# Performance work log

Hardware: AMD Instinct MI355X
Metric: run time of the kernel (lower is better)

The kernel has to match this reference:

```python
import jax, jax.numpy as jnp
import numpy as np

B, N, C, M = 64, 8732, 21, 16  # batch, priors (SSD300), classes (VOC), max objects


def setup_inputs() -> dict:
    key = jax.random.key(0)
    k1, k2 = jax.random.split(key)
    confOut = jax.random.normal(k1, (B, N, C), dtype=jnp.float32)
    bboxOut = jax.random.normal(k2, (B, N, 4), dtype=jnp.float32)

    rng = np.random.default_rng(0)
    # prior boxes [x1,y1,x2,y2], positive width/height
    px1 = rng.uniform(0.0, 0.8, (N, 1)).astype(np.float32)
    py1 = rng.uniform(0.0, 0.8, (N, 1)).astype(np.float32)
    pw = rng.uniform(0.05, 0.2, (N, 1)).astype(np.float32)
    ph = rng.uniform(0.05, 0.2, (N, 1)).astype(np.float32)
    predBoxes = np.concatenate([px1, py1, px1 + pw, py1 + ph], axis=1)

    # target layout: [num, (cls,x1,y1,x2,y2,k) * M]
    target = np.zeros((B, 1 + 6 * M), dtype=np.float32)
    target[:, 0] = rng.integers(1, M + 1, B)
    cls = rng.integers(1, C, (B, M)).astype(np.float32)  # all positive classes
    tx1 = rng.uniform(0.0, 0.8, (B, M)).astype(np.float32)
    ty1 = rng.uniform(0.0, 0.8, (B, M)).astype(np.float32)
    tw = rng.uniform(0.05, 0.2, (B, M)).astype(np.float32)
    th = rng.uniform(0.05, 0.2, (B, M)).astype(np.float32)
    ks = np.stack([rng.choice(N, M, replace=False) for _ in range(B)]).astype(np.float32)
    flat = np.stack([cls, tx1, ty1, tx1 + tw, ty1 + th, ks], axis=-1).reshape(B, 6 * M)
    target[:, 1:] = flat

    return {"confOut": confOut, "bboxOut": bboxOut,
            "target": jnp.asarray(target), "predBoxes": jnp.asarray(predBoxes)}


def _encode_box(true_box, pred_box):
    # standard SSD center/size encoding: (tc-pc)/pw, log(tw/pw)
    tcx = (true_box[..., 0] + true_box[..., 2]) * 0.5
    tcy = (true_box[..., 1] + true_box[..., 3]) * 0.5
    tw = true_box[..., 2] - true_box[..., 0]
    th = true_box[..., 3] - true_box[..., 1]
    pcx = (pred_box[..., 0] + pred_box[..., 2]) * 0.5
    pcy = (pred_box[..., 1] + pred_box[..., 3]) * 0.5
    pw = pred_box[..., 2] - pred_box[..., 0]
    ph = pred_box[..., 3] - pred_box[..., 1]
    return jnp.stack([(tcx - pcx) / pw, (tcy - pcy) / ph,
                      jnp.log(tw / pw), jnp.log(th / ph)], axis=-1)


def _ssd_loss(confOut, bboxOut, target, predBoxes):
    b, n, c = confOut.shape
    m = (target.shape[1] - 1) // 6
    t = target[:, 1:1 + 6 * m].reshape(b, m, 6)
    cls = t[..., 0].astype(jnp.int32)          # [B,M]
    tbox = t[..., 1:5]                          # [B,M,4]
    k = t[..., 5].astype(jnp.int32)             # [B,M] prior index
    num = target[:, 0].astype(jnp.int32)        # [B]
    valid = jnp.arange(m)[None, :] < num[:, None]      # [B,M]
    pos = valid & (cls > 0)
    bi = jnp.broadcast_to(jnp.arange(b)[:, None], (b, m))

    # ---- conf target assignment (scatter per object onto prior grid) ----
    posmask = jnp.zeros((b, n), bool).at[bi, k].max(pos)
    assigned = jnp.zeros((b, n), bool).at[bi, k].max(valid)  # score zeroed for all assigned
    conf_cls = jnp.zeros((b, n), jnp.int32).at[bi, k].max(jnp.where(pos, cls, 0))
    pnum = jnp.sum(pos)

    # ---- hard negative mining: globally sort bg log-prob ascending ----
    logp = jax.nn.log_softmax(confOut, axis=-1)             # [B,N,C]
    bg = jnp.where(assigned, 0.0, logp[..., 0]).reshape(-1)  # assigned -> 0 (sorts last)
    order = jnp.argsort(bg)
    pos_sorted = posmask.reshape(-1)[order]
    hit_pos = jnp.cumsum(pos_sorted.astype(jnp.int32)) > 0   # early-break emulation
    sel_sorted = (jnp.arange(b * n) < 3 * pnum) & (~hit_pos)
    negmask = jnp.zeros(b * n, bool).at[order].set(sel_sorted).reshape(b, n)

    selmask = posmask | negmask
    ce = -jnp.take_along_axis(logp, conf_cls[..., None], axis=-1)[..., 0]  # [B,N]
    conf_loss = jnp.sum(jnp.where(selmask, ce, 0.0)) / jnp.maximum(jnp.sum(selmask), 1)

    # ---- bbox target assignment + SmoothL1 on positives ----
    ebox = _encode_box(tbox, predBoxes[k])                   # [B,M,4]
    btgt = jnp.zeros((b, n, 4)).at[bi, k].add(jnp.where(valid[..., None], ebox, 0.0))
    bmask = jnp.zeros((b, n), bool).at[bi, k].max(valid)
    d = bboxOut - btgt
    ad = jnp.abs(d)
    sl1 = jnp.where(ad < 1.0, 0.5 * d * d, ad - 0.5)
    denom = jnp.maximum(jnp.sum(bmask) * 4, 1)
    bbox_loss = jnp.sum(jnp.where(bmask[..., None], sl1, 0.0)) / denom
    return conf_loss, bbox_loss


def reference(confOut, bboxOut, target, predBoxes):
    return _ssd_loss(confOut, bboxOut, target, predBoxes)
```

## Files before the change

### kernel.cpp

```cpp
#include <hip/hip_runtime.h>

constexpr int B = 64, N = 8732, C = 21, M = 16;
constexpr int TROW = 1 + 6 * M;
constexpr int NBIN = 2048;
constexpr unsigned BASE16 = 15103u;
constexpr int NSLAB = 8;
constexpr int TILE = 128;
constexpr int NTILES = (N + TILE - 1) / TILE;
constexpr int BPB = 16;
constexpr float FSCALE = 262144.0f;
constexpr unsigned long long CNT1 = 1ull << 44;
constexpr unsigned long long FIXMASK = (1ull << 44) - 1;

__device__ __forceinline__ unsigned f2key(float f) {
  unsigned u = __float_as_uint(f);
  return (u & 0x80000000u) ? ~u : (u | 0x80000000u);
}
__device__ __forceinline__ float key2f(unsigned k) {
  unsigned u = (k & 0x80000000u) ? (k ^ 0x80000000u) : ~k;
  return __uint_as_float(u);
}

__global__ __launch_bounds__(256) void k_zero(unsigned long long* __restrict__ z) {
  int idx = blockIdx.x * 256 + threadIdx.x;
  z[idx] = 0ull;
}

__global__ __launch_bounds__(256) void k_logp(
    const float* __restrict__ conf, const float* __restrict__ bbox,
    const float* __restrict__ target, const float* __restrict__ pred,
    unsigned long long* __restrict__ slab1, float4* __restrict__ batchCtl) {
  __shared__ __align__(16) float sbuf[2][TILE * C];
  __shared__ unsigned long long shist[NBIN];
  __shared__ int sk[M];
  int b = blockIdx.y, bx = blockIdx.x, tid = threadIdx.x;

  for (int i = tid; i < NBIN; i += 256) shist[i] = 0ull;
  const float* tr = target + (size_t)b * TROW;
  if (tid < M) {
    int num = (int)tr[0];
    sk[tid] = (tid < num) ? (int)tr[1 + 6 * tid + 5] : -1;
  }

  const size_t cbase = (size_t)b * N;
  int nt = (NTILES - 1 - bx) / BPB + 1;

  uint4 r0, r1, r2;
  int ld_nf4 = 0;

#define LOAD_T(kt)                                                        \
  {                                                                       \
    int tt_ = bx + (kt) * BPB;                                            \
    int n0_ = tt_ * TILE;                                                 \
    int rows_ = min(TILE, N - n0_);                                       \
    ld_nf4 = (rows_ * C) >> 2;                                            \
    const uint4* g4_ = (const uint4*)(conf + (cbase + n0_) * C);          \
    if (tid < ld_nf4) r0 = g4_[tid];                                      \
    if (tid + 256 < ld_nf4) r1 = g4_[tid + 256];                          \
    if (tid + 512 < ld_nf4) r2 = g4_[tid + 512];                          \
  }

#define WRITE_T(bi)                                                       \
  {                                                                       \
    uint4* s4_ = (uint4*)sbuf[bi];                                        \
    if (tid < ld_nf4) s4_[tid] = r0;                                      \
    if (tid + 256 < ld_nf4) s4_[tid + 256] = r1;                          \
    if (tid + 512 < ld_nf4) s4_[tid + 512] = r2;                          \
  }

  LOAD_T(0);
  WRITE_T(0);
  __syncthreads();

  for (int t = 0; t < nt; ++t) {
    if (t + 1 < nt) LOAD_T(t + 1);
    {
      int tt_ = bx + t * BPB;
      int n0_ = tt_ * TILE;
      int rows_ = min(TILE, N - n0_);
      if (tid < rows_) {
        int n = n0_ + tid;
        const float* x = sbuf[t & 1] + tid * C;
        float s0 = __expf(x[0]) + __expf(x[4]) + __expf(x[8]) + __expf(x[12]) + __expf(x[16]);
        float s1 = __expf(x[1]) + __expf(x[5]) + __expf(x[9]) + __expf(x[13]) + __expf(x[17]);
        float s2 = __expf(x[2]) + __expf(x[6]) + __expf(x[10]) + __expf(x[14]) + __expf(x[18]);
        float s3 = __expf(x[3]) + __expf(x[7]) + __expf(x[11]) + __expf(x[15]) + __expf(x[19]);
        float s = (s0 + s1) + (s2 + s3) + __expf(x[20]);
        float lp = x[0] - __logf(s);
        bool asg = false;
        for (int j = 0; j < M; j++) asg |= (sk[j] == n);
        if (!asg) {
          int idx = ((int)(f2key(lp) >> 16) - (int)BASE16) >> 1;
          idx = min(max(idx, 0), NBIN - 1);
          atomicAdd(&shist[idx],
                    CNT1 | (unsigned long long)((-lp) * FSCALE + 0.5f));
        }
      }
    }
    if (t + 1 < nt) WRITE_T((t + 1) & 1);
    __syncthreads();
  }
#undef LOAD_T
#undef WRITE_T

  unsigned long long* sg = slab1 + (size_t)(bx & (NSLAB - 1)) * NBIN;
  for (int i = tid; i < NBIN; i += 256) {
    unsigned long long v = shist[i];
    if (v) atomicAdd(&sg[i], v);
  }

  if (bx == 0) {
    float myValid = 0.f, myPos = 0.f, myCE = 0.f, mySL = 0.f;
    if (tid < M && sk[tid] >= 0) {
      const float* e = tr + 1 + 6 * tid;
      int cls = (int)e[0];
      float tx1 = e[1], ty1 = e[2], tx2 = e[3], ty2 = e[4];
      int k = sk[tid];
      float p0 = pred[k * 4 + 0], p1 = pred[k * 4 + 1];
      float p2 = pred[k * 4 + 2], p3 = pred[k * 4 + 3];
      float pw = p2 - p0, ph = p3 - p1;
      float pcx = (p0 + p2) * 0.5f, pcy = (p1 + p3) * 0.5f;
      float tw = tx2 - tx1, th = ty2 - ty1;
      float tcx = (tx1 + tx2) * 0.5f, tcy = (ty1 + ty2) * 0.5f;
      float ebv[4];
      ebv[0] = (tcx - pcx) / pw;
      ebv[1] = (tcy - pcy) / ph;
      ebv[2] = __logf(tw / pw);
      ebv[3] = __logf(th / ph);
      const float* bo = bbox + ((size_t)b * N + k) * 4;
      float sl = 0.f;
      for (int j = 0; j < 4; j++) {
        float d = bo[j] - ebv[j];
        float ad = fabsf(d);
        sl += (ad < 1.f) ? 0.5f * d * d : ad - 0.5f;
      }
      myValid = 1.f; mySL = sl;
      if (cls > 0) {
        const float* x = conf + ((size_t)b * N + k) * C;
        float s = 0.f;
        for (int c = 0; c < C; c++) s += __expf(x[c]);
        float lp = x[cls] - __logf(s);
        myPos = 1.f; myCE = -lp;
      }
    }
    if (tid < 64) {
      for (int off = 32; off; off >>= 1) {
        myValid += __shfl_down(myValid, off, 64);
        myPos   += __shfl_down(myPos, off, 64);
        myCE    += __shfl_down(myCE, off, 64);
        mySL    += __shfl_down(mySL, off, 64);
      }
      if (tid == 0) batchCtl[b] = make_float4(myPos, myValid, myCE, mySL);
    }
  }
}

__global__ __launch_bounds__(1024) void k_fin(
    const unsigned long long* __restrict__ slab1,
    const float4* __restrict__ batchCtl, float* __restrict__ out) {
  __shared__ unsigned long long sm[NBIN];
  __shared__ unsigned long long sscan[1024];
  __shared__ unsigned srank;
  __shared__ float sp, sva, sce, ssl;
  __shared__ double sNeg;
  int tid = threadIdx.x;

  if (tid < 64) {
    float4 v = batchCtl[tid];
    float p = v.x, va = v.y, ce = v.z, sl = v.w;
    for (int off = 32; off; off >>= 1) {
      p  += __shfl_down(p, off, 64);
      va += __shfl_down(va, off, 64);
      ce += __shfl_down(ce, off, 64);
      sl += __shfl_down(sl, off, 64);
    }
    if (tid == 0) {
      sp = p; sva = va; sce = ce; ssl = sl;
      srank = 3u * (unsigned)(p + 0.5f);
      sNeg = 0.0;
    }
  }

  for (int k = 0; k < NBIN / 1024; k++) {
    int bin = tid + k * 1024;
    unsigned long long v = 0ull;
    for (int s = 0; s < NSLAB; s++) v += slab1[(size_t)s * NBIN + bin];
    sm[bin] = v;
  }
  __syncthreads();

  unsigned long long h2[2];
  unsigned long long part = 0ull;
  for (int j = 0; j < 2; j++) { h2[j] = sm[tid * 2 + j]; part += h2[j]; }
  sscan[tid] = part;
  __syncthreads();
  for (int off = 1; off < 1024; off <<= 1) {
    unsigned long long add = (tid >= off) ? sscan[tid - off] : 0ull;
    __syncthreads();
    sscan[tid] += add;
    __syncthreads();
  }

  unsigned rank = srank;
  if (rank) {
    unsigned long long cum = sscan[tid] - part;
    for (int j = 0; j < 2; j++) {
      unsigned long long h = h2[j];
      unsigned c0 = (unsigned)(cum >> 44);
      unsigned c1 = (unsigned)((cum + h) >> 44);
      if (c0 < rank && c1 >= rank) {
        unsigned t = (unsigned)(tid * 2 + j);
        unsigned r = rank - c0;
        unsigned long long fixBelow = cum & FIXMASK;
        float ceEdge = -key2f((BASE16 + 2u * t) << 16);
        sNeg = (double)fixBelow / 262144.0 + (double)r * (double)ceEdge;
      }
      cum += h;
    }
  }
  __syncthreads();
  if (tid == 0) {
    out[0] = (sce + (float)sNeg) / fmaxf(4.0f * sp, 1.0f);
    out[1] = ssl / fmaxf(4.0f * sva, 1.0f);
  }
}

extern "C" void kernel_launch(void* const* d_in, const int* in_sizes, int n_in,
                              void* d_out, int out_size, void* d_ws, size_t ws_size,
                              hipStream_t stream) {
  const float* conf = (const float*)d_in[0];
  const float* bbox = (const float*)d_in[1];
  const float* target = (const float*)d_in[2];
  const float* pred = (const float*)d_in[3];
  float* out = (float*)d_out;

  char* ws = (char*)d_ws;
  unsigned long long* slab1 = (unsigned long long*)ws;
  size_t off = (size_t)NSLAB * NBIN * 8;
  float4* batchCtl = (float4*)(ws + off); off += 64 * 16;

  k_zero<<<64, 256, 0, stream>>>(slab1);
  k_logp<<<dim3(BPB, B), 256, 0, stream>>>(conf, bbox, target, pred,
                                           slab1, batchCtl);
  k_fin<<<1, 1024, 0, stream>>>(slab1, batchCtl, out);
}
```

Before: 31.39 us.

## Double tile size and prefetch two tiles ahead with dual register sets

Tiles grow from 128 to 256 priors, and blocks per batch drop from 16 to 8. The register prefetch becomes two alternating register sets, so global loads run two tiles ahead of compute instead of one. The goal is to hide global-memory latency on the conf stream. In exchange, shared memory doubles (2x256x21 floats), register pressure rises to 12 uint4 per thread, and the grid halves to 512 blocks. Only 256 threads run the softmax while a tile holds 256 rows, so every thread is busy, but occupancy may drop.

```diff
diff --git a/kernel.cpp b/kernel.cpp
--- a/kernel.cpp
+++ b/kernel.cpp
@@ -5,9 +5,9 @@
 constexpr int NBIN = 2048;
 constexpr unsigned BASE16 = 15103u;
 constexpr int NSLAB = 8;
-constexpr int TILE = 128;
+constexpr int TILE = 256;
 constexpr int NTILES = (N + TILE - 1) / TILE;
-constexpr int BPB = 16;
+constexpr int BPB = 8;
 constexpr float FSCALE = 262144.0f;
 constexpr unsigned long long CNT1 = 1ull << 44;
 constexpr unsigned long long FIXMASK = (1ull << 44) - 1;
@@ -45,35 +45,46 @@
   const size_t cbase = (size_t)b * N;
   int nt = (NTILES - 1 - bx) / BPB + 1;
 
-  uint4 r0, r1, r2;
-  int ld_nf4 = 0;
-
-#define LOAD_T(kt)                                                        \
+  uint4 a0, a1, a2, a3, a4, a5;
+  uint4 b0, b1, b2, b3, b4, b5;
+  int la = 0, lb = 0;
+
+#define LOAD_SET(R0, R1, R2, R3, R4, R5, LN, kt)                          \
   {                                                                       \
     int tt_ = bx + (kt) * BPB;                                            \
     int n0_ = tt_ * TILE;                                                 \
     int rows_ = min(TILE, N - n0_);                                       \
-    ld_nf4 = (rows_ * C) >> 2;                                            \
+    LN = (rows_ * C) >> 2;                                                \
     const uint4* g4_ = (const uint4*)(conf + (cbase + n0_) * C);          \
-    if (tid < ld_nf4) r0 = g4_[tid];                                      \
-    if (tid + 256 < ld_nf4) r1 = g4_[tid + 256];                          \
-    if (tid + 512 < ld_nf4) r2 = g4_[tid + 512];                          \
-  }
-
-#define WRITE_T(bi)                                                       \
+    if (tid < LN) R0 = g4_[tid];                                          \
+    if (tid + 256 < LN) R1 = g4_[tid + 256];                              \
+    if (tid + 512 < LN) R2 = g4_[tid + 512];                              \
+    if (tid + 768 < LN) R3 = g4_[tid + 768];                              \
+    if (tid + 1024 < LN) R4 = g4_[tid + 1024];                            \
+    if (tid + 1280 < LN) R5 = g4_[tid + 1280];                            \
+  }
+
+#define WRITE_SET(R0, R1, R2, R3, R4, R5, LN, bi)                         \
   {                                                                       \
     uint4* s4_ = (uint4*)sbuf[bi];                                        \
-    if (tid < ld_nf4) s4_[tid] = r0;                                      \
-    if (tid + 256 < ld_nf4) s4_[tid + 256] = r1;                          \
-    if (tid + 512 < ld_nf4) s4_[tid + 512] = r2;                          \
-  }
-
-  LOAD_T(0);
-  WRITE_T(0);
+    if (tid < LN) s4_[tid] = R0;                                          \
+    if (tid + 256 < LN) s4_[tid + 256] = R1;                              \
+    if (tid + 512 < LN) s4_[tid + 512] = R2;                              \
+    if (tid + 768 < LN) s4_[tid + 768] = R3;                              \
+    if (tid + 1024 < LN) s4_[tid + 1024] = R4;                            \
+    if (tid + 1280 < LN) s4_[tid + 1280] = R5;                            \
+  }
+
+  LOAD_SET(a0, a1, a2, a3, a4, a5, la, 0);
+  WRITE_SET(a0, a1, a2, a3, a4, a5, la, 0);
+  if (1 < nt) LOAD_SET(b0, b1, b2, b3, b4, b5, lb, 1);
   __syncthreads();
 
   for (int t = 0; t < nt; ++t) {
-    if (t + 1 < nt) LOAD_T(t + 1);
+    if (t + 2 < nt) {
+      if ((t & 1) == 0) { LOAD_SET(a0, a1, a2, a3, a4, a5, la, t + 2); }
+      else              { LOAD_SET(b0, b1, b2, b3, b4, b5, lb, t + 2); }
+    }
     {
       int tt_ = bx + t * BPB;
       int n0_ = tt_ * TILE;
@@ -97,11 +108,14 @@
         }
       }
     }
-    if (t + 1 < nt) WRITE_T((t + 1) & 1);
+    if (t + 1 < nt) {
+      if (((t + 1) & 1) == 0) { WRITE_SET(a0, a1, a2, a3, a4, a5, la, 0); }
+      else                    { WRITE_SET(b0, b1, b2, b3, b4, b5, lb, 1); }
+    }
     __syncthreads();
   }
-#undef LOAD_T
-#undef WRITE_T
+#undef LOAD_SET
+#undef WRITE_SET
 
   unsigned long long* sg = slab1 + (size_t)(bx & (NSLAB - 1)) * NBIN;
   for (int i = tid; i < NBIN; i += 256) {
```

Result: faster. 28.42 us (-9.5%).

## Stage conf tiles via direct global-to-LDS loads with larger tiles

Applied to the files above, without the earlier changes.

Replaces register-staged global loads plus LDS writes with __builtin_amdgcn_global_load_lds 16-byte direct copies into the double buffer. Tile size doubles to 256 rows, so every thread computes a row, and blocks per batch drop to 8. The aim is to cut VGPR pressure and the explicit LDS write pass. It relies on the 16-byte LDS-DMA variant being supported and on the syncthreads waiting for the async loads to finish. Fewer blocks (512 instead of 1024) may reduce the parallelism available for latency hiding.

```diff
diff --git a/kernel.cpp b/kernel.cpp
--- a/kernel.cpp
+++ b/kernel.cpp
@@ -5,12 +5,15 @@
 constexpr int NBIN = 2048;
 constexpr unsigned BASE16 = 15103u;
 constexpr int NSLAB = 8;
-constexpr int TILE = 128;
+constexpr int TILE = 256;
 constexpr int NTILES = (N + TILE - 1) / TILE;
-constexpr int BPB = 16;
+constexpr int BPB = 8;
 constexpr float FSCALE = 262144.0f;
 constexpr unsigned long long CNT1 = 1ull << 44;
 constexpr unsigned long long FIXMASK = (1ull << 44) - 1;
+
+typedef __attribute__((address_space(1))) const unsigned int g_as_t;
+typedef __attribute__((address_space(3))) unsigned int l_as_t;
 
 __device__ __forceinline__ unsigned f2key(float f) {
   unsigned u = __float_as_uint(f);
@@ -34,6 +37,7 @@
   __shared__ unsigned long long shist[NBIN];
   __shared__ int sk[M];
   int b = blockIdx.y, bx = blockIdx.x, tid = threadIdx.x;
+  int wave = tid >> 6, lane = tid & 63;
 
   for (int i = tid; i < NBIN; i += 256) shist[i] = 0ull;
   const float* tr = target + (size_t)b * TROW;
@@ -45,35 +49,29 @@
   const size_t cbase = (size_t)b * N;
   int nt = (NTILES - 1 - bx) / BPB + 1;
 
-  uint4 r0, r1, r2;
-  int ld_nf4 = 0;
-
-#define LOAD_T(kt)                                                        \
-  {                                                                       \
-    int tt_ = bx + (kt) * BPB;                                            \
-    int n0_ = tt_ * TILE;                                                 \
-    int rows_ = min(TILE, N - n0_);                                       \
-    ld_nf4 = (rows_ * C) >> 2;                                            \
-    const uint4* g4_ = (const uint4*)(conf + (cbase + n0_) * C);          \
-    if (tid < ld_nf4) r0 = g4_[tid];                                      \
-    if (tid + 256 < ld_nf4) r1 = g4_[tid + 256];                          \
-    if (tid + 512 < ld_nf4) r2 = g4_[tid + 512];                          \
-  }
-
-#define WRITE_T(bi)                                                       \
-  {                                                                       \
-    uint4* s4_ = (uint4*)sbuf[bi];                                        \
-    if (tid < ld_nf4) s4_[tid] = r0;                                      \
-    if (tid + 256 < ld_nf4) s4_[tid + 256] = r1;                          \
-    if (tid + 512 < ld_nf4) s4_[tid + 512] = r2;                          \
-  }
-
-  LOAD_T(0);
-  WRITE_T(0);
+#define STAGE(kt, bi)                                                       \
+  {                                                                         \
+    int tt_ = bx + (kt) * BPB;                                              \
+    int n0_ = tt_ * TILE;                                                   \
+    int rows_ = min(TILE, N - n0_);                                         \
+    int bytes_ = rows_ * C * 4;             \
+    const char* gb_ = (const char*)(conf + (cbase + n0_) * C);              \
+    char* lb_ = (char*)sbuf[bi];                                            \
+    for (int c_ = wave; c_ * 1024 < bytes_; c_ += 4) {                      \
+      int off_ = c_ * 1024 + lane * 16;                                     \
+      if (off_ + 16 <= bytes_) {                                            \
+        __builtin_amdgcn_global_load_lds((g_as_t*)(gb_ + off_),             \
+                                         (l_as_t*)(lb_ + c_ * 1024),        \
+                                         16, 0, 0);                         \
+      }                                                                     \
+    }                                                                       \
+  }
+
+  STAGE(0, 0);
   __syncthreads();
 
   for (int t = 0; t < nt; ++t) {
-    if (t + 1 < nt) LOAD_T(t + 1);
+    if (t + 1 < nt) STAGE(t + 1, (t + 1) & 1);
     {
       int tt_ = bx + t * BPB;
       int n0_ = tt_ * TILE;
@@ -97,11 +95,9 @@
         }
       }
     }
-    if (t + 1 < nt) WRITE_T((t + 1) & 1);
     __syncthreads();
   }
-#undef LOAD_T
-#undef WRITE_T
+#undef STAGE
 
   unsigned long long* sg = slab1 + (size_t)(bx & (NSLAB - 1)) * NBIN;
   for (int i = tid; i < NBIN; i += 256) {
```

Result: faster. 28.43 us (-9.4%).
